# Kernel optimization log

Hardware: AMD Instinct MI355X
Metric: run time of the kernel (lower is better)

Reference implementation:

```python
import math
import jax, jax.numpy as jnp
import numpy as np

N_HEADS = 32
N_KV_HEADS = 8
HEAD_DIM = 128
DIM = 4096
B = 32
MAX_SEQ = 4096
Q_LEN = 1
START_POS = 4095


def setup_inputs() -> dict:
    key = jax.random.key(0)
    ks = jax.random.split(key, 9)
    x = jax.random.normal(ks[0], (B, Q_LEN, DIM), dtype=jnp.float32)
    # RoPE angles for the current positions (seqlen=Q_LEN, half head_dim pairs)
    inv_freq = 1.0 / (500000.0 ** (np.arange(0, HEAD_DIM, 2, dtype=np.float32) / HEAD_DIM))
    pos = np.arange(START_POS, START_POS + Q_LEN, dtype=np.float32)
    ang = pos[:, None] * inv_freq[None, :]  # [Q_LEN, HEAD_DIM//2]
    freqs_cos = jnp.asarray(np.cos(ang), dtype=jnp.float32)
    freqs_sin = jnp.asarray(np.sin(ang), dtype=jnp.float32)
    cache_k = jax.random.normal(ks[1], (B, MAX_SEQ, N_KV_HEADS, HEAD_DIM), dtype=jnp.float32)
    cache_v = jax.random.normal(ks[2], (B, MAX_SEQ, N_KV_HEADS, HEAD_DIM), dtype=jnp.float32)
    s = 0.02
    wq = jax.random.normal(ks[3], (N_HEADS * HEAD_DIM, DIM), dtype=jnp.float32) * s
    wk = jax.random.normal(ks[4], (N_KV_HEADS * HEAD_DIM, DIM), dtype=jnp.float32) * s
    wv = jax.random.normal(ks[5], (N_KV_HEADS * HEAD_DIM, DIM), dtype=jnp.float32) * s
    wo = jax.random.normal(ks[6], (DIM, N_HEADS * HEAD_DIM), dtype=jnp.float32) * s
    return {"x": x, "start_pos": START_POS, "freqs_cos": freqs_cos, "freqs_sin": freqs_sin,
            "cache_k": cache_k, "cache_v": cache_v, "wq": wq, "wk": wk, "wv": wv, "wo": wo}


def _rope(t, cos, sin):
    # t: [B, S, h, hd]; cos/sin: [S, hd//2]; complex multiply on (even, odd) pairs
    tr = t.reshape(*t.shape[:-1], HEAD_DIM // 2, 2)
    a, b = tr[..., 0], tr[..., 1]
    c = cos[None, :, None, :]
    s = sin[None, :, None, :]
    out = jnp.stack([a * c - b * s, a * s + b * c], axis=-1)
    return out.reshape(t.shape)


def reference(x, start_pos, freqs_cos, freqs_sin, cache_k, cache_v, wq, wk, wv, wo):
    bsz, seqlen, _ = x.shape
    n_rep = N_HEADS // N_KV_HEADS
    xq = jnp.einsum('bsd,od->bso', x, wq).reshape(bsz, seqlen, N_HEADS, HEAD_DIM)
    xk = jnp.einsum('bsd,od->bso', x, wk).reshape(bsz, seqlen, N_KV_HEADS, HEAD_DIM)
    xv = jnp.einsum('bsd,od->bso', x, wv).reshape(bsz, seqlen, N_KV_HEADS, HEAD_DIM)
    xq = _rope(xq, freqs_cos, freqs_sin)
    xk = _rope(xk, freqs_cos, freqs_sin)
    # KV-cache update (start_pos is a static Python int)
    cache_k = cache_k.at[:, start_pos:start_pos + seqlen].set(xk)
    cache_v = cache_v.at[:, start_pos:start_pos + seqlen].set(xv)
    keys = cache_k[:, :start_pos + seqlen]    # [B, T, Hkv, hd]
    values = cache_v[:, :start_pos + seqlen]  # [B, T, Hkv, hd]
    # GQA: group query heads [H] -> [Hkv, n_rep]; avoids materializing repeated KV
    q = xq.reshape(bsz, seqlen, N_KV_HEADS, n_rep, HEAD_DIM)
    scale = 1.0 / math.sqrt(HEAD_DIM)
    scores = jnp.einsum('bsgrd,btgd->bgrst', q, keys) * scale  # [B, Hkv, n_rep, S, T]
    probs = jax.nn.softmax(scores, axis=-1)
    out = jnp.einsum('bgrst,btgd->bsgrd', probs, values)
    out = out.reshape(bsz, seqlen, N_HEADS * HEAD_DIM)
    return jnp.einsum('bse,de->bsd', out, wo)
```

## Files before the change

kernel.cpp:

```cpp
#include <hip/hip_runtime.h>

#define B_    32
#define DIM_  4096
#define NH_   32
#define NKV_  8
#define HD_   128
#define TSEQ  4096
#define NQKV  6144
#define GSPLIT 32
#define BK    32
#define NT    128
#define KRANGE (DIM_ / GSPLIT)
#define KTILES (KRANGE / BK)
#define TSPL  32
#define TS    128

typedef float f4_t __attribute__((ext_vector_type(4)));

__device__ __forceinline__ f4_t ntl(const float* p) {
    return __builtin_nontemporal_load((const f4_t*)p);
}

__global__ __launch_bounds__(256) void gemm32(
    const float* __restrict__ A, const float* __restrict__ w0,
    const float* __restrict__ w1, const float* __restrict__ w2,
    int b1, int b2, int N, float* __restrict__ po)
{
    __shared__ __align__(16) float wt[BK][NT + 4];
    __shared__ __align__(16) float xp[KRANGE][33];
    const int tid = threadIdx.x;
    const int cg  = tid & 31;
    const int bg  = tid >> 5;
    const int ct  = blockIdx.x * NT;
    const int k0  = blockIdx.y * KRANGE;

    const float* wb_; int c0_;
    if (ct < b1)      { wb_ = w0; c0_ = ct; }
    else if (ct < b2) { wb_ = w1; c0_ = ct - b1; }
    else              { wb_ = w2; c0_ = ct - b2; }

    const int kqx = (tid & 31) * 4;
    const int rrx = tid >> 5;
    const int kq2 = (tid & 7) * 4;
    const int rr2 = tid >> 3;

    f4_t wreg[4];

    #pragma unroll
    for (int st = 0; st < 4; ++st) {
        const int bb = st * 8 + rrx;
        const f4_t xv = *(const f4_t*)(A + (size_t)bb * DIM_ + k0 + kqx);
        xp[kqx + 0][bb] = xv[0]; xp[kqx + 1][bb] = xv[1];
        xp[kqx + 2][bb] = xv[2]; xp[kqx + 3][bb] = xv[3];
    }
    #pragma unroll
    for (int st = 0; st < 4; ++st)
        wreg[st] = ntl(wb_ + (size_t)(c0_ + st * 32 + rr2) * DIM_ + k0 + kq2);
    #pragma unroll
    for (int st = 0; st < 4; ++st) {
        const int c = st * 32 + rr2;
        wt[kq2 + 0][c] = wreg[st][0]; wt[kq2 + 1][c] = wreg[st][1];
        wt[kq2 + 2][c] = wreg[st][2]; wt[kq2 + 3][c] = wreg[st][3];
    }
    __syncthreads();

    float acc[4][4];
    #pragma unroll
    for (int i = 0; i < 4; ++i)
        #pragma unroll
        for (int j = 0; j < 4; ++j) acc[i][j] = 0.f;

    for (int tt = 0; tt < KTILES; ++tt) {
        if (tt < KTILES - 1) {
            #pragma unroll
            for (int st = 0; st < 4; ++st)
                wreg[st] = ntl(wb_ + (size_t)(c0_ + st * 32 + rr2) * DIM_
                               + k0 + (tt + 1) * BK + kq2);
        }
        #pragma unroll 8
        for (int kk = 0; kk < BK; ++kk) {
            const int kr = tt * BK + kk;
            const float4 xa = *(const float4*)&xp[kr][bg * 4];
            const float4 wa = *(const float4*)&wt[kk][cg * 4];
            const float xv[4] = {xa.x, xa.y, xa.z, xa.w};
            const float wv[4] = {wa.x, wa.y, wa.z, wa.w};
            #pragma unroll
            for (int i = 0; i < 4; ++i)
                #pragma unroll
                for (int j = 0; j < 4; ++j)
                    acc[i][j] = fmaf(xv[i], wv[j], acc[i][j]);
        }
        __syncthreads();
        if (tt < KTILES - 1) {
            #pragma unroll
            for (int st = 0; st < 4; ++st) {
                const int c = st * 32 + rr2;
                wt[kq2 + 0][c] = wreg[st][0]; wt[kq2 + 1][c] = wreg[st][1];
                wt[kq2 + 2][c] = wreg[st][2]; wt[kq2 + 3][c] = wreg[st][3];
            }
            __syncthreads();
        }
    }

    const size_t srow = (size_t)blockIdx.y * B_;
    #pragma unroll
    for (int i = 0; i < 4; ++i) {
        const int b = bg * 4 + i;
        const float4 o = make_float4(acc[i][0], acc[i][1], acc[i][2], acc[i][3]);
        *(float4*)&po[(srow + b) * N + ct + cg * 4] = o;
    }
}

__global__ void reduce_rope(const float* __restrict__ po,
                            const float* __restrict__ fc, const float* __restrict__ fs,
                            float* __restrict__ qkv)
{
    const int pid = blockIdx.x * 256 + threadIdx.x;
    const int b  = pid / (NQKV / 4);
    const int c0 = (pid - b * (NQKV / 4)) * 4;
    f4_t v = {0.f, 0.f, 0.f, 0.f};
    #pragma unroll
    for (int s = 0; s < GSPLIT; ++s)
        v += *(const f4_t*)(po + ((size_t)s * B_ + b) * NQKV + c0);
    if (c0 < DIM_ + NKV_ * HD_) {
        const int i = (c0 & 127) >> 1;
        const float ca = fc[i],     sa = fs[i];
        const float cb = fc[i + 1], sb = fs[i + 1];
        f4_t o;
        o[0] = v[0] * ca - v[1] * sa;
        o[1] = v[0] * sa + v[1] * ca;
        o[2] = v[2] * cb - v[3] * sb;
        o[3] = v[2] * sb + v[3] * cb;
        v = o;
    }
    *(f4_t*)(qkv + (size_t)b * NQKV + c0) = v;
}

__device__ __forceinline__ void attn_step(const f4_t kc, const f4_t vc,
                                          const f4_t* q, f4_t* acc, float* l)
{
    float p0 = kc[0]*q[0][0] + kc[1]*q[0][1] + kc[2]*q[0][2] + kc[3]*q[0][3];
    float p1 = kc[0]*q[1][0] + kc[1]*q[1][1] + kc[2]*q[1][2] + kc[3]*q[1][3];
    float p2 = kc[0]*q[2][0] + kc[1]*q[2][1] + kc[2]*q[2][2] + kc[3]*q[2][3];
    float p3 = kc[0]*q[3][0] + kc[1]*q[3][1] + kc[2]*q[3][2] + kc[3]*q[3][3];
    #pragma unroll
    for (int off = 1; off < 32; off <<= 1) {
        p0 += __shfl_xor(p0, off);
        p1 += __shfl_xor(p1, off);
        p2 += __shfl_xor(p2, off);
        p3 += __shfl_xor(p3, off);
    }
    const float scale = 0.08838834764831845f;
    p0 = __expf(p0 * scale); p1 = __expf(p1 * scale);
    p2 = __expf(p2 * scale); p3 = __expf(p3 * scale);
    l[0] += p0; l[1] += p1; l[2] += p2; l[3] += p3;
    acc[0] += p0 * vc; acc[1] += p1 * vc;
    acc[2] += p2 * vc; acc[3] += p3 * vc;
}

__global__ __launch_bounds__(256) void attn_partial(
    const float* __restrict__ qkv, const float* __restrict__ ck,
    const float* __restrict__ cv,
    float* __restrict__ po , float* __restrict__ pl )
{
    const int blk = blockIdx.x;
    const int s = blk & (TSPL - 1);
    const int b = blk / TSPL;
    const int tid  = threadIdx.x;
    const int g    = tid >> 5;
    const int lane = tid & 31;
    const int d4   = lane * 4;
    const float* qb = qkv + (size_t)b * NQKV;

    f4_t q[4];
    #pragma unroll
    for (int h = 0; h < 4; ++h)
        q[h] = *(const f4_t*)(qb + (g * 4 + h) * HD_ + d4);

    f4_t zero4 = {0.f, 0.f, 0.f, 0.f};
    f4_t acc[4] = {zero4, zero4, zero4, zero4};
    float l[4] = {0.f, 0.f, 0.f, 0.f};

    const int t0 = s * TS;
    const bool last = (s == TSPL - 1);
    const int niter = TS - (last ? 1 : 0);

    const size_t base = ((size_t)b * TSEQ + t0) * (NKV_ * HD_) + tid * 4;
    const float* kp = ck + base;
    const float* vp = cv + base;
    const int step = NKV_ * HD_;

    f4_t kc = ntl(kp), vc = ntl(vp);
    kp += step; vp += step;
    f4_t k1 = ntl(kp), v1 = ntl(vp);
    for (int it = 0; it < niter - 2; ++it) {
        kp += step; vp += step;
        const f4_t k2 = ntl(kp);
        const f4_t v2 = ntl(vp);
        attn_step(kc, vc, q, acc, l);
        kc = k1; vc = v1; k1 = k2; v1 = v2;
    }
    attn_step(kc, vc, q, acc, l);
    attn_step(k1, v1, q, acc, l);
    if (last) {
        const f4_t kf = *(const f4_t*)(qb + DIM_ + tid * 4);
        const f4_t vf = *(const f4_t*)(qb + DIM_ + NKV_ * HD_ + tid * 4);
        attn_step(kf, vf, q, acc, l);
    }

    float* pob = po + (((size_t)(b * NKV_ + g) * TSPL) + s) * 512;
    #pragma unroll
    for (int h = 0; h < 4; ++h)
        *(f4_t*)&pob[h * HD_ + d4] = acc[h];
    if (lane == 0) {
        float* plb = pl + ((size_t)(b * NKV_ + g) * TSPL + s) * 4;
        plb[0] = l[0]; plb[1] = l[1]; plb[2] = l[2]; plb[3] = l[3];
    }
}

__global__ void attn_combine(const float* __restrict__ po, const float* __restrict__ pl,
                             float* __restrict__ ao)
{
    const int bg  = blockIdx.x;
    const int tid = threadIdx.x;
    const int e0  = tid * 4;
    const int r   = e0 >> 7;
    f4_t o = {0.f, 0.f, 0.f, 0.f};
    float ls = 0.f;
    #pragma unroll 8
    for (int s = 0; s < TSPL; ++s) {
        o += *(const f4_t*)&po[((size_t)bg * TSPL + s) * 512 + e0];
        ls += pl[((size_t)bg * TSPL + s) * 4 + r];
    }
    o *= (1.f / ls);
    const int b = bg >> 3, g = bg & 7;
    *(f4_t*)&ao[(size_t)b * DIM_ + g * 512 + e0] = o;
}

__global__ void reduce_out(const float* __restrict__ po, float* __restrict__ out)
{
    const int pid = blockIdx.x * 256 + threadIdx.x;
    const int b  = pid >> 10;
    const int c0 = (pid & 1023) * 4;
    f4_t v = {0.f, 0.f, 0.f, 0.f};
    #pragma unroll
    for (int s = 0; s < GSPLIT; ++s)
        v += *(const f4_t*)(po + ((size_t)s * B_ + b) * DIM_ + c0);
    *(f4_t*)(out + (size_t)b * DIM_ + c0) = v;
}

extern "C" void kernel_launch(void* const* d_in, const int* in_sizes, int n_in,
                              void* d_out, int out_size, void* d_ws, size_t ws_size,
                              hipStream_t stream)
{
    (void)in_sizes; (void)n_in; (void)out_size; (void)ws_size;
    const float* x  = (const float*)d_in[0];
    const float* fc = (const float*)d_in[2];
    const float* fs = (const float*)d_in[3];
    const float* ck = (const float*)d_in[4];
    const float* cv = (const float*)d_in[5];
    const float* wq = (const float*)d_in[6];
    const float* wk = (const float*)d_in[7];
    const float* wv = (const float*)d_in[8];
    const float* wo = (const float*)d_in[9];
    float* out = (float*)d_out;
    float* ws  = (float*)d_ws;

    float* qkv  = ws;
    float* aout = ws + 196608;
    float* apo  = ws + 327680;
    float* apl  = ws + 4521984;
    float* gp   = ws + 4554752;

    gemm32<<<dim3(NQKV / NT, GSPLIT), 256, 0, stream>>>(
        x, wq, wk, wv, DIM_, DIM_ + NKV_ * HD_, NQKV, gp);
    reduce_rope<<<dim3(B_ * (NQKV / 4) / 256), 256, 0, stream>>>(gp, fc, fs, qkv);
    attn_partial<<<dim3(B_ * TSPL), 256, 0, stream>>>(qkv, ck, cv, apo, apl);
    attn_combine<<<dim3(B_ * NKV_), 128, 0, stream>>>(apo, apl, aout);
    gemm32<<<dim3(DIM_ / NT, GSPLIT), 256, 0, stream>>>(
        aout, wo, wo, wo, DIM_, DIM_, DIM_, gp);
    reduce_out<<<dim3(B_ * DIM_ / 4 / 256), 256, 0, stream>>>(gp, out);
}
```

Baseline: 249.2 us.

## Load weights directly from global into registers, dropping LDS weight staging

The skinny GEMM kernel no longer stages weight tiles through shared memory with double-buffered registers and per-tile barriers. Each thread now reads its own four weight rows straight from global memory with nontemporal float4 loads and multiplies them against the shared activation tile. This removes LDS writes, bank traffic and __syncthreads in the K loop. In exchange, a wavefront's loads hit 32 different rows 16 bytes at a time, so global coalescing is worse and latency hiding relies on unrolling rather than explicit prefetch.

```diff
diff --git a/kernel.cpp b/kernel.cpp
--- a/kernel.cpp
+++ b/kernel.cpp
@@ -8,10 +8,8 @@
 #define TSEQ  4096
 #define NQKV  6144
 #define GSPLIT 32
-#define BK    32
 #define NT    128
 #define KRANGE (DIM_ / GSPLIT)
-#define KTILES (KRANGE / BK)
 #define TSPL  32
 #define TS    128
 
@@ -26,7 +24,6 @@
     const float* __restrict__ w1, const float* __restrict__ w2,
     int b1, int b2, int N, float* __restrict__ po)
 {
-    __shared__ __align__(16) float wt[BK][NT + 4];
     __shared__ __align__(16) float xp[KRANGE][33];
     const int tid = threadIdx.x;
     const int cg  = tid & 31;
@@ -39,30 +36,23 @@
     else if (ct < b2) { wb_ = w1; c0_ = ct - b1; }
     else              { wb_ = w2; c0_ = ct - b2; }
 
-    const int kqx = (tid & 31) * 4;
-    const int rrx = tid >> 5;
-    const int kq2 = (tid & 7) * 4;
-    const int rr2 = tid >> 3;
-
-    f4_t wreg[4];
-
-    #pragma unroll
-    for (int st = 0; st < 4; ++st) {
-        const int bb = st * 8 + rrx;
-        const f4_t xv = *(const f4_t*)(A + (size_t)bb * DIM_ + k0 + kqx);
-        xp[kqx + 0][bb] = xv[0]; xp[kqx + 1][bb] = xv[1];
-        xp[kqx + 2][bb] = xv[2]; xp[kqx + 3][bb] = xv[3];
-    }
-    #pragma unroll
-    for (int st = 0; st < 4; ++st)
-        wreg[st] = ntl(wb_ + (size_t)(c0_ + st * 32 + rr2) * DIM_ + k0 + kq2);
-    #pragma unroll
-    for (int st = 0; st < 4; ++st) {
-        const int c = st * 32 + rr2;
-        wt[kq2 + 0][c] = wreg[st][0]; wt[kq2 + 1][c] = wreg[st][1];
-        wt[kq2 + 2][c] = wreg[st][2]; wt[kq2 + 3][c] = wreg[st][3];
+    {
+        const int kqx = (tid & 31) * 4;
+        const int rrx = tid >> 5;
+        #pragma unroll
+        for (int st = 0; st < 4; ++st) {
+            const int bb = st * 8 + rrx;
+            const f4_t xv = *(const f4_t*)(A + (size_t)bb * DIM_ + k0 + kqx);
+            xp[kqx + 0][bb] = xv[0]; xp[kqx + 1][bb] = xv[1];
+            xp[kqx + 2][bb] = xv[2]; xp[kqx + 3][bb] = xv[3];
+        }
     }
     __syncthreads();
+
+    const float* wr0 = wb_ + (size_t)(c0_ + cg * 4 + 0) * DIM_ + k0;
+    const float* wr1 = wb_ + (size_t)(c0_ + cg * 4 + 1) * DIM_ + k0;
+    const float* wr2 = wb_ + (size_t)(c0_ + cg * 4 + 2) * DIM_ + k0;
+    const float* wr3 = wb_ + (size_t)(c0_ + cg * 4 + 3) * DIM_ + k0;
 
     float acc[4][4];
     #pragma unroll
@@ -70,35 +60,23 @@
         #pragma unroll
         for (int j = 0; j < 4; ++j) acc[i][j] = 0.f;
 
-    for (int tt = 0; tt < KTILES; ++tt) {
-        if (tt < KTILES - 1) {
-            #pragma unroll
-            for (int st = 0; st < 4; ++st)
-                wreg[st] = ntl(wb_ + (size_t)(c0_ + st * 32 + rr2) * DIM_
-                               + k0 + (tt + 1) * BK + kq2);
-        }
-        #pragma unroll 8
-        for (int kk = 0; kk < BK; ++kk) {
-            const int kr = tt * BK + kk;
-            const float4 xa = *(const float4*)&xp[kr][bg * 4];
-            const float4 wa = *(const float4*)&wt[kk][cg * 4];
+    #pragma unroll 4
+    for (int kq = 0; kq < KRANGE / 4; ++kq) {
+        f4_t w[4];
+        w[0] = ntl(wr0 + kq * 4);
+        w[1] = ntl(wr1 + kq * 4);
+        w[2] = ntl(wr2 + kq * 4);
+        w[3] = ntl(wr3 + kq * 4);
+        #pragma unroll
+        for (int kk = 0; kk < 4; ++kk) {
+            const int k = kq * 4 + kk;
+            const float4 xa = *(const float4*)&xp[k][bg * 4];
             const float xv[4] = {xa.x, xa.y, xa.z, xa.w};
-            const float wv[4] = {wa.x, wa.y, wa.z, wa.w};
             #pragma unroll
             for (int i = 0; i < 4; ++i)
                 #pragma unroll
                 for (int j = 0; j < 4; ++j)
-                    acc[i][j] = fmaf(xv[i], wv[j], acc[i][j]);
-        }
-        __syncthreads();
-        if (tt < KTILES - 1) {
-            #pragma unroll
-            for (int st = 0; st < 4; ++st) {
-                const int c = st * 32 + rr2;
-                wt[kq2 + 0][c] = wreg[st][0]; wt[kq2 + 1][c] = wreg[st][1];
-                wt[kq2 + 2][c] = wreg[st][2]; wt[kq2 + 3][c] = wreg[st][3];
-            }
-            __syncthreads();
+                    acc[i][j] = fmaf(xv[i], w[j][kk], acc[i][j]);
         }
     }
 
```

After: 605.8 us. 2.43x slower.
